# Optimization experiments

Measured on AMD Instinct MI355X. Metric: run time of the kernel, lower is better.

The kernel has to match this reference:

```python
import jax, jax.numpy as jnp
import numpy as np

SIGMA = 1.0
NUM_LAYERS = 1
B, N, D, CD = 4, 256, 128, 3


def setup_inputs() -> dict:
    key = jax.random.key(0)
    ks = jax.random.split(key, 10)
    s = lambda fan_in: 1.0 / np.sqrt(fan_in)
    return {
        "local_emb": jax.random.normal(ks[0], (B, N, D), dtype=jnp.float32),
        "coords": jax.random.normal(ks[1], (B, N, CD), dtype=jnp.float32),
        # msg_mlp: Linear(2D -> D), ReLU, Linear(D -> D). Weights stored [in, out].
        "mW1": jax.random.uniform(ks[2], (2 * D, D), jnp.float32, -s(2 * D), s(2 * D)),
        "mb1": jax.random.uniform(ks[3], (D,), jnp.float32, -s(2 * D), s(2 * D)),
        "mW2": jax.random.uniform(ks[4], (D, D), jnp.float32, -s(D), s(D)),
        "mb2": jax.random.uniform(ks[5], (D,), jnp.float32, -s(D), s(D)),
        # update_mlp: Linear(D+CD -> D), ReLU, Linear(D -> D)
        "uW1": jax.random.uniform(ks[6], (D + CD, D), jnp.float32, -s(D + CD), s(D + CD)),
        "ub1": jax.random.uniform(ks[7], (D,), jnp.float32, -s(D + CD), s(D + CD)),
        "uW2": jax.random.uniform(ks[8], (D, D), jnp.float32, -s(D), s(D)),
        "ub2": jax.random.uniform(ks[9], (D,), jnp.float32, -s(D), s(D)),
    }


def reference(local_emb, coords, mW1, mb1, mW2, mb2, uW1, ub1, uW2, ub2):
    # Split msg_mlp first layer: Linear(concat([h_i, h_j])) == h_i @ W1a + h_j @ W1b
    W1a, W1b = mW1[:D], mW1[D:]
    for _ in range(NUM_LAYERS):
        # Gaussian affinity A[b,i,j] = exp(-||c_i - c_j||^2 / (2 sigma^2))
        diff = coords[:, :, None, :] - coords[:, None, :, :]        # [B,N,N,CD]
        dist2 = jnp.sum(diff * diff, axis=-1)                        # [B,N,N]
        A = jnp.exp(-dist2 / (2.0 * SIGMA ** 2))
        # Pairwise message MLP: pre[b,i,j,:] = h_i W1a + h_j W1b + b1
        pre = (jnp.einsum("bid,de->bie", local_emb, W1a)[:, :, None, :]
               + jnp.einsum("bjd,de->bje", local_emb, W1b)[:, None, :, :]
               + mb1)                                                # [B,N,N,D]
        msgs = jnp.einsum("bijd,de->bije", jax.nn.relu(pre), mW2) + mb2
        # Gaussian-weighted aggregation
        agg = jnp.einsum("bij,bijd->bid", A, msgs)                   # [B,N,D]
        # Update MLP on [agg, coords]
        upd_in = jnp.concatenate([agg, coords], axis=-1)             # [B,N,D+CD]
        delta = jax.nn.relu(upd_in @ uW1 + ub1) @ uW2 + ub2
        local_emb = local_emb + delta
    return local_emb
```

## Files before the change

### kernel.cpp

```cpp
#include <hip/hip_runtime.h>
#include <math.h>

#define NN 256
#define DD 128

typedef float4 f4;

#define FMA4(acc, s, v)                          \
  acc.x = fmaf(s, v.x, acc.x);                   \
  acc.y = fmaf(s, v.y, acc.y);                   \
  acc.z = fmaf(s, v.z, acc.z);                   \
  acc.w = fmaf(s, v.w, acc.w);

#define FMA4R(acc, a, p, v)                              \
  acc.x = fmaf(a, fmaxf(p.x + v.x, 0.f), acc.x);         \
  acc.y = fmaf(a, fmaxf(p.y + v.y, 0.f), acc.y);         \
  acc.z = fmaf(a, fmaxf(p.z + v.z, 0.f), acc.z);         \
  acc.w = fmaf(a, fmaxf(p.w + v.w, 0.f), acc.w);

#define ZERO4 {0.f, 0.f, 0.f, 0.f}

__global__ __launch_bounds__(512, 2) void h1_kernel(
    const float* __restrict__ emb,
    const float* __restrict__ mW1,
    const float* __restrict__ mb1,
    float* __restrict__ H1a,
    float* __restrict__ H1b)
{
    const int tid  = threadIdx.x;
    const int row0 = blockIdx.x * 4;

    __shared__ f4 embT[DD];
    __shared__ f4 red[8 * 4 * 64];

    {
        const int r = tid >> 7, k = tid & 127;
        const float v = emb[(size_t)(row0 + r) * DD + k];
        ((float*)embT)[k * 4 + r] = v;
    }
    __syncthreads();

    const int cq    = tid & 63;
    const int kh    = tid >> 6;
    const int wq    = cq & 31;
    const int wrow0 = (cq < 32) ? 0 : DD;
    const f4* __restrict__ W4 = (const f4*)mW1;

    f4 w[16];
    #pragma unroll
    for (int t = 0; t < 16; ++t)
        w[t] = W4[(size_t)(wrow0 + kh * 16 + t) * 32 + wq];

    f4 a0 = ZERO4, a1 = ZERO4, a2 = ZERO4, a3 = ZERO4;
    #pragma unroll
    for (int t = 0; t < 16; ++t) {
        const f4 e4 = embT[kh * 16 + t];
        FMA4(a0, e4.x, w[t]);
        FMA4(a1, e4.y, w[t]);
        FMA4(a2, e4.z, w[t]);
        FMA4(a3, e4.w, w[t]);
    }
    red[(kh * 4 + 0) * 64 + cq] = a0;
    red[(kh * 4 + 1) * 64 + cq] = a1;
    red[(kh * 4 + 2) * 64 + cq] = a2;
    red[(kh * 4 + 3) * 64 + cq] = a3;
    __syncthreads();

    const float* __restrict__ redF = (const float*)red;
    #pragma unroll
    for (int t = 0; t < 2; ++t) {
        const int o  = t * 512 + tid;
        const int rr = o >> 8, oc = o & 255;
        float v = 0.f;
        #pragma unroll
        for (int q = 0; q < 8; ++q) v += redF[q * 1024 + rr * 256 + oc];
        if (oc < DD) H1a[(size_t)(row0 + rr) * DD + oc]        = v + mb1[oc];
        else         H1b[(size_t)(row0 + rr) * DD + (oc - DD)] = v;
    }
}

__global__ __launch_bounds__(512, 2) void gnn_kernel(
    const float* __restrict__ emb,
    const float* __restrict__ coords,
    const float* __restrict__ mW2, const float* __restrict__ mb2,
    const float* __restrict__ uW1, const float* __restrict__ ub1,
    const float* __restrict__ uW2, const float* __restrict__ ub2,
    const float* __restrict__ H1a, const float* __restrict__ H1b,
    float* __restrict__ out)
{
    const int tid  = threadIdx.x;
    const int row0 = blockIdx.x * 4;
    const int b    = row0 >> 8;
    const int i0   = row0 & 255;

    __shared__ float cS[NN * 3];
    __shared__ f4 As4[NN];
    __shared__ f4 red[16 * 4 * 32];
    __shared__ f4 R_T[DD];
    __shared__ f4 U_T[DD + 3];
    __shared__ f4 h_T[DD];
    __shared__ f4 sAs4[16];
    __shared__ float sAtot[4];

    const int eq = tid & 31;
    const int js = tid >> 5;

    const f4* __restrict__ Ha4 = (const f4*)(H1a + (size_t)row0 * DD);
    const f4 pa0 = Ha4[0 * 32 + eq];
    const f4 pa1 = Ha4[1 * 32 + eq];
    const f4 pa2 = Ha4[2 * 32 + eq];
    const f4 pa3 = Ha4[3 * 32 + eq];

    const float* __restrict__ cb = coords + (size_t)b * NN * 3;
    if (tid < 192) ((f4*)cS)[tid] = ((const f4*)cb)[tid];
    __syncthreads();

    {
        const int j = tid & 255, rA = tid >> 8;
        const float cjx = cS[j * 3], cjy = cS[j * 3 + 1], cjz = cS[j * 3 + 2];
        float* __restrict__ AsF = (float*)As4;
        {
            const int ii = i0 + rA;
            const float dx = cjx - cS[ii * 3], dy = cjy - cS[ii * 3 + 1], dz = cjz - cS[ii * 3 + 2];
            AsF[j * 4 + rA] = __expf(-0.5f * (dx * dx + dy * dy + dz * dz));
        }
        {
            const int ii = i0 + rA + 2;
            const float dx = cjx - cS[ii * 3], dy = cjy - cS[ii * 3 + 1], dz = cjz - cS[ii * 3 + 2];
            AsF[j * 4 + rA + 2] = __expf(-0.5f * (dx * dx + dy * dy + dz * dz));
        }
    }
    __syncthreads();

    const f4* __restrict__ Hb4 = (const f4*)(H1b + (size_t)b * NN * DD);
    f4 v[16];
    #pragma unroll
    for (int t = 0; t < 16; ++t) v[t] = Hb4[(size_t)(js * 16 + t) * 32 + eq];

    f4 a0 = ZERO4, a1 = ZERO4, a2 = ZERO4, a3 = ZERO4, sA4 = ZERO4;
    #pragma unroll
    for (int t = 0; t < 16; ++t) {
        const f4 a = As4[js * 16 + t];
        sA4.x += a.x; sA4.y += a.y; sA4.z += a.z; sA4.w += a.w;
        FMA4R(a0, a.x, pa0, v[t]);
        FMA4R(a1, a.y, pa1, v[t]);
        FMA4R(a2, a.z, pa2, v[t]);
        FMA4R(a3, a.w, pa3, v[t]);
    }
    red[js * 128 + 0 * 32 + eq] = a0;
    red[js * 128 + 1 * 32 + eq] = a1;
    red[js * 128 + 2 * 32 + eq] = a2;
    red[js * 128 + 3 * 32 + eq] = a3;
    if (eq == 0) sAs4[js] = sA4;
    __syncthreads();

    const float* __restrict__ redF = (const float*)red;
    {
        const int r = tid >> 7, e = tid & 127;
        float s = 0.f;
        #pragma unroll
        for (int q = 0; q < 16; ++q) s += redF[q * 512 + r * 128 + e];
        ((float*)R_T)[e * 4 + r] = s;
    }
    if (tid < 4) {
        const float* __restrict__ sF = (const float*)sAs4;
        float s = 0.f;
        #pragma unroll
        for (int q = 0; q < 16; ++q) s += sF[q * 4 + tid];
        sAtot[tid] = s;
    }
    __syncthreads();

    const int cq = eq, kh = js;
    const f4* __restrict__ W2g = (const f4*)mW2;
    {
        f4 wv[8];
        #pragma unroll
        for (int t = 0; t < 8; ++t) wv[t] = W2g[(size_t)(kh * 8 + t) * 32 + cq];
        f4 g0 = ZERO4, g1 = ZERO4, g2 = ZERO4, g3 = ZERO4;
        #pragma unroll
        for (int t = 0; t < 8; ++t) {
            const f4 rv = R_T[kh * 8 + t];
            FMA4(g0, rv.x, wv[t]);
            FMA4(g1, rv.y, wv[t]);
            FMA4(g2, rv.z, wv[t]);
            FMA4(g3, rv.w, wv[t]);
        }
        red[kh * 128 + 0 * 32 + cq] = g0;
        red[kh * 128 + 1 * 32 + cq] = g1;
        red[kh * 128 + 2 * 32 + cq] = g2;
        red[kh * 128 + 3 * 32 + cq] = g3;
    }
    __syncthreads();

    {
        const int r = tid >> 7, e = tid & 127;
        const float m2 = mb2[e];
        float s = sAtot[r] * m2;
        #pragma unroll
        for (int q = 0; q < 16; ++q) s += redF[q * 512 + r * 128 + e];
        ((float*)U_T)[e * 4 + r] = s;
    }
    if (tid < 12) {
        const int r = tid & 3, c = tid >> 2;
        ((float*)U_T)[(DD + c) * 4 + r] = cS[(i0 + r) * 3 + c];
    }
    __syncthreads();

    const f4* __restrict__ U1g = (const f4*)uW1;
    {
        f4 wv[8];
        #pragma unroll
        for (int t = 0; t < 8; ++t) wv[t] = U1g[(size_t)(kh * 8 + t) * 32 + cq];
        f4 g0 = ZERO4, g1 = ZERO4, g2 = ZERO4, g3 = ZERO4;
        #pragma unroll
        for (int t = 0; t < 8; ++t) {
            const f4 uv = U_T[kh * 8 + t];
            FMA4(g0, uv.x, wv[t]);
            FMA4(g1, uv.y, wv[t]);
            FMA4(g2, uv.z, wv[t]);
            FMA4(g3, uv.w, wv[t]);
        }
        if (kh == 15) {
            #pragma unroll
            for (int t = 0; t < 3; ++t) {
                const f4 wt = U1g[(size_t)(DD + t) * 32 + cq];
                const f4 uv = U_T[DD + t];
                FMA4(g0, uv.x, wt);
                FMA4(g1, uv.y, wt);
                FMA4(g2, uv.z, wt);
                FMA4(g3, uv.w, wt);
            }
        }
        red[kh * 128 + 0 * 32 + cq] = g0;
        red[kh * 128 + 1 * 32 + cq] = g1;
        red[kh * 128 + 2 * 32 + cq] = g2;
        red[kh * 128 + 3 * 32 + cq] = g3;
    }
    __syncthreads();

    {
        const int r = tid >> 7, e = tid & 127;
        float s = ub1[e];
        #pragma unroll
        for (int q = 0; q < 16; ++q) s += redF[q * 512 + r * 128 + e];
        ((float*)h_T)[e * 4 + r] = fmaxf(s, 0.f);
    }
    __syncthreads();

    const f4* __restrict__ U2g = (const f4*)uW2;
    {
        f4 wv[8];
        #pragma unroll
        for (int t = 0; t < 8; ++t) wv[t] = U2g[(size_t)(kh * 8 + t) * 32 + cq];
        f4 g0 = ZERO4, g1 = ZERO4, g2 = ZERO4, g3 = ZERO4;
        #pragma unroll
        for (int t = 0; t < 8; ++t) {
            const f4 hv = h_T[kh * 8 + t];
            FMA4(g0, hv.x, wv[t]);
            FMA4(g1, hv.y, wv[t]);
            FMA4(g2, hv.z, wv[t]);
            FMA4(g3, hv.w, wv[t]);
        }
        red[kh * 128 + 0 * 32 + cq] = g0;
        red[kh * 128 + 1 * 32 + cq] = g1;
        red[kh * 128 + 2 * 32 + cq] = g2;
        red[kh * 128 + 3 * 32 + cq] = g3;
    }
    __syncthreads();

    {
        const int r = tid >> 7, e = tid & 127;
        float s = ub2[e];
        #pragma unroll
        for (int q = 0; q < 16; ++q) s += redF[q * 512 + r * 128 + e];
        out[(size_t)(row0 + r) * DD + e] = emb[(size_t)(row0 + r) * DD + e] + s;
    }
}

extern "C" void kernel_launch(void* const* d_in, const int* in_sizes, int n_in,
                              void* d_out, int out_size, void* d_ws, size_t ws_size,
                              hipStream_t stream) {
    const float* emb    = (const float*)d_in[0];
    const float* coords = (const float*)d_in[1];
    const float* mW1    = (const float*)d_in[2];
    const float* mb1    = (const float*)d_in[3];
    const float* mW2    = (const float*)d_in[4];
    const float* mb2    = (const float*)d_in[5];
    const float* uW1    = (const float*)d_in[6];
    const float* ub1    = (const float*)d_in[7];
    const float* uW2    = (const float*)d_in[8];
    const float* ub2    = (const float*)d_in[9];
    float* out = (float*)d_out;

    float* H1a = (float*)d_ws;
    float* H1b = H1a + 4 * NN * DD;

    h1_kernel<<<dim3(256), dim3(512), 0, stream>>>(emb, mW1, mb1, H1a, H1b);
    gnn_kernel<<<dim3(256), dim3(512), 0, stream>>>(
        emb, coords, mW2, mb2, uW1, ub1, uW2, ub2, H1a, H1b, out);
}
```

Baseline: 82.34 us.

## Fuse H1 projection into GNN kernel with a software grid barrier

Merges the two kernels into one persistent launch. Each block computes its H1a rows into shared memory and its H1b rows into global memory. A global atomic-counter barrier then makes all H1b rows visible before the pairwise aggregation, and the affinity computation is overlapped with the H1 stage. This removes one kernel launch and the H1a global round-trip. In exchange it adds a memset launch and depends on all 256 blocks being co-resident; without that guarantee the spin barrier can deadlock.

```diff
diff --git a/kernel.cpp b/kernel.cpp
--- a/kernel.cpp
+++ b/kernel.cpp
@@ -3,6 +3,7 @@
 
 #define NN 256
 #define DD 128
+#define GRID 256
 
 typedef float4 f4;
 
@@ -20,72 +21,15 @@
 
 #define ZERO4 {0.f, 0.f, 0.f, 0.f}
 
-__global__ __launch_bounds__(512, 2) void h1_kernel(
-    const float* __restrict__ emb,
-    const float* __restrict__ mW1,
-    const float* __restrict__ mb1,
-    float* __restrict__ H1a,
-    float* __restrict__ H1b)
-{
-    const int tid  = threadIdx.x;
-    const int row0 = blockIdx.x * 4;
-
-    __shared__ f4 embT[DD];
-    __shared__ f4 red[8 * 4 * 64];
-
-    {
-        const int r = tid >> 7, k = tid & 127;
-        const float v = emb[(size_t)(row0 + r) * DD + k];
-        ((float*)embT)[k * 4 + r] = v;
-    }
-    __syncthreads();
-
-    const int cq    = tid & 63;
-    const int kh    = tid >> 6;
-    const int wq    = cq & 31;
-    const int wrow0 = (cq < 32) ? 0 : DD;
-    const f4* __restrict__ W4 = (const f4*)mW1;
-
-    f4 w[16];
-    #pragma unroll
-    for (int t = 0; t < 16; ++t)
-        w[t] = W4[(size_t)(wrow0 + kh * 16 + t) * 32 + wq];
-
-    f4 a0 = ZERO4, a1 = ZERO4, a2 = ZERO4, a3 = ZERO4;
-    #pragma unroll
-    for (int t = 0; t < 16; ++t) {
-        const f4 e4 = embT[kh * 16 + t];
-        FMA4(a0, e4.x, w[t]);
-        FMA4(a1, e4.y, w[t]);
-        FMA4(a2, e4.z, w[t]);
-        FMA4(a3, e4.w, w[t]);
-    }
-    red[(kh * 4 + 0) * 64 + cq] = a0;
-    red[(kh * 4 + 1) * 64 + cq] = a1;
-    red[(kh * 4 + 2) * 64 + cq] = a2;
-    red[(kh * 4 + 3) * 64 + cq] = a3;
-    __syncthreads();
-
-    const float* __restrict__ redF = (const float*)red;
-    #pragma unroll
-    for (int t = 0; t < 2; ++t) {
-        const int o  = t * 512 + tid;
-        const int rr = o >> 8, oc = o & 255;
-        float v = 0.f;
-        #pragma unroll
-        for (int q = 0; q < 8; ++q) v += redF[q * 1024 + rr * 256 + oc];
-        if (oc < DD) H1a[(size_t)(row0 + rr) * DD + oc]        = v + mb1[oc];
-        else         H1b[(size_t)(row0 + rr) * DD + (oc - DD)] = v;
-    }
-}
-
-__global__ __launch_bounds__(512, 2) void gnn_kernel(
+__global__ __launch_bounds__(512, 2) void fused_gnn(
     const float* __restrict__ emb,
     const float* __restrict__ coords,
+    const float* __restrict__ mW1, const float* __restrict__ mb1,
     const float* __restrict__ mW2, const float* __restrict__ mb2,
     const float* __restrict__ uW1, const float* __restrict__ ub1,
     const float* __restrict__ uW2, const float* __restrict__ ub2,
-    const float* __restrict__ H1a, const float* __restrict__ H1b,
+    float* __restrict__ H1b,
+    unsigned* __restrict__ bar,
     float* __restrict__ out)
 {
     const int tid  = threadIdx.x;
@@ -93,70 +37,121 @@
     const int b    = row0 >> 8;
     const int i0   = row0 & 255;
 
+    __shared__ f4 red[2048];
+    __shared__ f4 embT[DD];
     __shared__ float cS[NN * 3];
     __shared__ f4 As4[NN];
-    __shared__ f4 red[16 * 4 * 32];
+    __shared__ float HaS[4][DD];
     __shared__ f4 R_T[DD];
     __shared__ f4 U_T[DD + 3];
     __shared__ f4 h_T[DD];
     __shared__ f4 sAs4[16];
     __shared__ float sAtot[4];
 
+    const int cq1 = tid & 63;
+    const int kh1 = tid >> 6;
+    const int wq  = cq1 & 31;
+    const int wr0 = (cq1 < 32) ? 0 : DD;
+    const f4* __restrict__ W4 = (const f4*)mW1;
+
+    f4 w[16];
+    #pragma unroll
+    for (int t = 0; t < 16; ++t)
+        w[t] = W4[(size_t)(wr0 + kh1 * 16 + t) * 32 + wq];
+
+    {   const int r = tid >> 7, k = tid & 127;
+        ((float*)embT)[k * 4 + r] = emb[(size_t)(row0 + r) * DD + k]; }
+    const float* __restrict__ cb = coords + (size_t)b * NN * 3;
+    if (tid < 192) ((f4*)cS)[tid] = ((const f4*)cb)[tid];
+    __syncthreads();
+
+    {   const int j = tid & 255, rA = tid >> 8;
+        const float cjx = cS[j * 3], cjy = cS[j * 3 + 1], cjz = cS[j * 3 + 2];
+        float* __restrict__ AsF = (float*)As4;
+        {   const int ii = i0 + rA;
+            const float dx = cjx - cS[ii * 3], dy = cjy - cS[ii * 3 + 1], dz = cjz - cS[ii * 3 + 2];
+            AsF[j * 4 + rA] = __expf(-0.5f * (dx * dx + dy * dy + dz * dz)); }
+        {   const int ii = i0 + rA + 2;
+            const float dx = cjx - cS[ii * 3], dy = cjy - cS[ii * 3 + 1], dz = cjz - cS[ii * 3 + 2];
+            AsF[j * 4 + rA + 2] = __expf(-0.5f * (dx * dx + dy * dy + dz * dz)); }
+    }
+
+    {   f4 a0 = ZERO4, a1 = ZERO4, a2 = ZERO4, a3 = ZERO4;
+        #pragma unroll
+        for (int t = 0; t < 16; ++t) {
+            const f4 e4 = embT[kh1 * 16 + t];
+            FMA4(a0, e4.x, w[t]);
+            FMA4(a1, e4.y, w[t]);
+            FMA4(a2, e4.z, w[t]);
+            FMA4(a3, e4.w, w[t]);
+        }
+        red[(kh1 * 4 + 0) * 64 + cq1] = a0;
+        red[(kh1 * 4 + 1) * 64 + cq1] = a1;
+        red[(kh1 * 4 + 2) * 64 + cq1] = a2;
+        red[(kh1 * 4 + 3) * 64 + cq1] = a3;
+    }
+    __syncthreads();
+
+    {   const float* __restrict__ redF = (const float*)red;
+        #pragma unroll
+        for (int t = 0; t < 2; ++t) {
+            const int o  = t * 512 + tid;
+            const int rr = o >> 8, oc = o & 255;
+            float v = 0.f;
+            #pragma unroll
+            for (int q = 0; q < 8; ++q) v += redF[q * 1024 + rr * 256 + oc];
+            if (oc < DD) HaS[rr][oc] = v + mb1[oc];
+            else         H1b[(size_t)(row0 + rr) * DD + (oc - DD)] = v;
+        }
+    }
+
+    const int rr2 = tid >> 7, ea = tid & 127;
+    const float embv = emb[(size_t)(row0 + rr2) * DD + ea];
+    const float mb2v = mb2[ea], ub1v = ub1[ea], ub2v = ub2[ea];
+
+    __threadfence();
+    __syncthreads();
+    if (tid == 0) {
+        __hip_atomic_fetch_add(bar, 1u, __ATOMIC_RELEASE, __HIP_MEMORY_SCOPE_AGENT);
+        while (__hip_atomic_load(bar, __ATOMIC_RELAXED, __HIP_MEMORY_SCOPE_AGENT) < GRID)
+            __builtin_amdgcn_s_sleep(2);
+        __threadfence();
+    }
+    __syncthreads();
+
     const int eq = tid & 31;
     const int js = tid >> 5;
 
-    const f4* __restrict__ Ha4 = (const f4*)(H1a + (size_t)row0 * DD);
-    const f4 pa0 = Ha4[0 * 32 + eq];
-    const f4 pa1 = Ha4[1 * 32 + eq];
-    const f4 pa2 = Ha4[2 * 32 + eq];
-    const f4 pa3 = Ha4[3 * 32 + eq];
-
-    const float* __restrict__ cb = coords + (size_t)b * NN * 3;
-    if (tid < 192) ((f4*)cS)[tid] = ((const f4*)cb)[tid];
-    __syncthreads();
-
-    {
-        const int j = tid & 255, rA = tid >> 8;
-        const float cjx = cS[j * 3], cjy = cS[j * 3 + 1], cjz = cS[j * 3 + 2];
-        float* __restrict__ AsF = (float*)As4;
-        {
-            const int ii = i0 + rA;
-            const float dx = cjx - cS[ii * 3], dy = cjy - cS[ii * 3 + 1], dz = cjz - cS[ii * 3 + 2];
-            AsF[j * 4 + rA] = __expf(-0.5f * (dx * dx + dy * dy + dz * dz));
-        }
-        {
-            const int ii = i0 + rA + 2;
-            const float dx = cjx - cS[ii * 3], dy = cjy - cS[ii * 3 + 1], dz = cjz - cS[ii * 3 + 2];
-            AsF[j * 4 + rA + 2] = __expf(-0.5f * (dx * dx + dy * dy + dz * dz));
-        }
-    }
-    __syncthreads();
+    const f4 pa0 = ((const f4*)HaS[0])[eq];
+    const f4 pa1 = ((const f4*)HaS[1])[eq];
+    const f4 pa2 = ((const f4*)HaS[2])[eq];
+    const f4 pa3 = ((const f4*)HaS[3])[eq];
 
     const f4* __restrict__ Hb4 = (const f4*)(H1b + (size_t)b * NN * DD);
     f4 v[16];
     #pragma unroll
     for (int t = 0; t < 16; ++t) v[t] = Hb4[(size_t)(js * 16 + t) * 32 + eq];
 
-    f4 a0 = ZERO4, a1 = ZERO4, a2 = ZERO4, a3 = ZERO4, sA4 = ZERO4;
-    #pragma unroll
-    for (int t = 0; t < 16; ++t) {
-        const f4 a = As4[js * 16 + t];
-        sA4.x += a.x; sA4.y += a.y; sA4.z += a.z; sA4.w += a.w;
-        FMA4R(a0, a.x, pa0, v[t]);
-        FMA4R(a1, a.y, pa1, v[t]);
-        FMA4R(a2, a.z, pa2, v[t]);
-        FMA4R(a3, a.w, pa3, v[t]);
-    }
-    red[js * 128 + 0 * 32 + eq] = a0;
-    red[js * 128 + 1 * 32 + eq] = a1;
-    red[js * 128 + 2 * 32 + eq] = a2;
-    red[js * 128 + 3 * 32 + eq] = a3;
-    if (eq == 0) sAs4[js] = sA4;
+    {   f4 a0 = ZERO4, a1 = ZERO4, a2 = ZERO4, a3 = ZERO4, sA4 = ZERO4;
+        #pragma unroll
+        for (int t = 0; t < 16; ++t) {
+            const f4 a = As4[js * 16 + t];
+            sA4.x += a.x; sA4.y += a.y; sA4.z += a.z; sA4.w += a.w;
+            FMA4R(a0, a.x, pa0, v[t]);
+            FMA4R(a1, a.y, pa1, v[t]);
+            FMA4R(a2, a.z, pa2, v[t]);
+            FMA4R(a3, a.w, pa3, v[t]);
+        }
+        red[js * 128 + 0 * 32 + eq] = a0;
+        red[js * 128 + 1 * 32 + eq] = a1;
+        red[js * 128 + 2 * 32 + eq] = a2;
+        red[js * 128 + 3 * 32 + eq] = a3;
+        if (eq == 0) sAs4[js] = sA4;
+    }
     __syncthreads();
 
     const float* __restrict__ redF = (const float*)red;
-    {
-        const int r = tid >> 7, e = tid & 127;
+    {   const int r = tid >> 7, e = tid & 127;
         float s = 0.f;
         #pragma unroll
         for (int q = 0; q < 16; ++q) s += redF[q * 512 + r * 128 + e];
@@ -172,8 +167,7 @@
     __syncthreads();
 
     const int cq = eq, kh = js;
-    const f4* __restrict__ W2g = (const f4*)mW2;
-    {
+    {   const f4* __restrict__ W2g = (const f4*)mW2;
         f4 wv[8];
         #pragma unroll
         for (int t = 0; t < 8; ++t) wv[t] = W2g[(size_t)(kh * 8 + t) * 32 + cq];
@@ -193,10 +187,8 @@
     }
     __syncthreads();
 
-    {
-        const int r = tid >> 7, e = tid & 127;
-        const float m2 = mb2[e];
-        float s = sAtot[r] * m2;
+    {   const int r = tid >> 7, e = tid & 127;
+        float s = sAtot[r] * mb2v;
         #pragma unroll
         for (int q = 0; q < 16; ++q) s += redF[q * 512 + r * 128 + e];
         ((float*)U_T)[e * 4 + r] = s;
@@ -207,8 +199,7 @@
     }
     __syncthreads();
 
-    const f4* __restrict__ U1g = (const f4*)uW1;
-    {
+    {   const f4* __restrict__ U1g = (const f4*)uW1;
         f4 wv[8];
         #pragma unroll
         for (int t = 0; t < 8; ++t) wv[t] = U1g[(size_t)(kh * 8 + t) * 32 + cq];
@@ -239,17 +230,15 @@
     }
     __syncthreads();
 
-    {
-        const int r = tid >> 7, e = tid & 127;
-        float s = ub1[e];
+    {   const int r = tid >> 7, e = tid & 127;
+        float s = ub1v;
         #pragma unroll
         for (int q = 0; q < 16; ++q) s += redF[q * 512 + r * 128 + e];
         ((float*)h_T)[e * 4 + r] = fmaxf(s, 0.f);
     }
     __syncthreads();
 
-    const f4* __restrict__ U2g = (const f4*)uW2;
-    {
+    {   const f4* __restrict__ U2g = (const f4*)uW2;
         f4 wv[8];
         #pragma unroll
         for (int t = 0; t < 8; ++t) wv[t] = U2g[(size_t)(kh * 8 + t) * 32 + cq];
@@ -269,12 +258,11 @@
     }
     __syncthreads();
 
-    {
-        const int r = tid >> 7, e = tid & 127;
-        float s = ub2[e];
-        #pragma unroll
-        for (int q = 0; q < 16; ++q) s += redF[q * 512 + r * 128 + e];
-        out[(size_t)(row0 + r) * DD + e] = emb[(size_t)(row0 + r) * DD + e] + s;
+    {   const int r = tid >> 7, e = tid & 127;
+        float s = ub2v;
+        #pragma unroll
+        for (int q = 0; q < 16; ++q) s += redF[q * 512 + r * 128 + e];
+        out[(size_t)(row0 + r) * DD + e] = embv + s;
     }
 }
 
@@ -293,10 +281,10 @@
     const float* ub2    = (const float*)d_in[9];
     float* out = (float*)d_out;
 
-    float* H1a = (float*)d_ws;
-    float* H1b = H1a + 4 * NN * DD;
-
-    h1_kernel<<<dim3(256), dim3(512), 0, stream>>>(emb, mW1, mb1, H1a, H1b);
-    gnn_kernel<<<dim3(256), dim3(512), 0, stream>>>(
-        emb, coords, mW2, mb2, uW1, ub1, uW2, ub2, H1a, H1b, out);
+    unsigned* bar = (unsigned*)d_ws;
+    float* H1b = (float*)((char*)d_ws + 256);
+
+    hipMemsetAsync(d_ws, 0, 256, stream);
+    fused_gnn<<<dim3(GRID), dim3(512), 0, stream>>>(
+        emb, coords, mW1, mb1, mW2, mb2, uW1, ub1, uW2, ub2, H1b, bar, out);
 }
```

Result: slower. 133.6 us (+62.3%).
